# Optimization experiments

Hardware: AMD Instinct MI355X
Metric: run time of the kernel (lower is better)

Reference implementation:

```python
import jax, jax.numpy as jnp
import numpy as np

B, IN, OUT, R, G = 1024, 4096, 4096, 16, 16
N_GROUPS = IN * OUT // G  # 1048576


def setup_inputs() -> dict:
    key = jax.random.key(0)
    k1, k2, k3, k4, k5 = jax.random.split(key, 5)
    x = jax.random.normal(k1, (B, IN), dtype=jnp.float32)
    # packed 4-bit weights: each int holds two nibbles (low | high<<4), values 0..255
    qweight = jax.random.randint(k2, (N_GROUPS, G // 2), 0, 256, dtype=jnp.int32)
    # positive per-group scale (original stores abs-max as fp16, used as fp32)
    scale_factor = jax.random.uniform(k3, (N_GROUPS, 1), dtype=jnp.float32, minval=0.01, maxval=1.0)
    # kaiming-normal-ish init for lora_a; lora_b nonzero for a non-degenerate baseline
    lora_a = jax.random.normal(k4, (R, IN), dtype=jnp.float32) * np.sqrt(2.0 / IN).astype(np.float32)
    lora_b = jax.random.normal(k5, (OUT, R), dtype=jnp.float32) * 0.01
    alpha = jnp.ones((1,), dtype=jnp.float32)
    return {"x": x, "qweight": qweight, "scale_factor": scale_factor,
            "lora_a": lora_a, "lora_b": lora_b, "alpha": alpha}


def _dequantize_4bit(qweight, scale_factor):
    # qweight: [n_groups, G/2] int32 packed nibbles; scale: [n_groups, 1]
    g, half = qweight.shape
    lo = qweight & 15            # even positions
    hi = (qweight >> 4) & 15     # odd positions
    q8 = jnp.stack([lo, hi], axis=-1).reshape(g, half * 2)  # interleave -> [n_groups, G]
    x_norm = q8.astype(jnp.float32) / 15.0
    return x_norm * 2.0 * scale_factor - scale_factor       # [n_groups, G]


def reference(x, qweight, scale_factor, lora_a, lora_b, alpha):
    # dequantize and view as (in_features, -1), matching weight.view(x.shape[1], -1)
    weight = _dequantize_4bit(qweight, scale_factor).reshape(x.shape[1], -1)  # [IN, OUT]
    base = jnp.einsum('bi,oi->bo', x, weight)  # F.linear(x, weight) = x @ weight.T
    lora = alpha * jnp.einsum('br,or->bo', jnp.einsum('bi,ri->br', x, lora_a), lora_b)
    return base + lora
```

## Files before the change

kernel.cpp:

```cpp
#include <hip/hip_runtime.h>

typedef __attribute__((ext_vector_type(2))) _Float16 h2;
typedef __attribute__((ext_vector_type(2))) __fp16 p2;
typedef __attribute__((ext_vector_type(8))) _Float16 f16x8;
typedef __attribute__((ext_vector_type(4))) float fv4;
typedef __attribute__((ext_vector_type(4))) int iv4;
typedef __attribute__((ext_vector_type(2))) int iv2;
typedef unsigned int u32;

#define K_IN 4096
#define N_OUT 4096
#define KE 4160

__global__ __launch_bounds__(256) void prep_all(
        const float* __restrict__ x, const float* __restrict__ la,
        const int* __restrict__ qw, const float* __restrict__ sc,
        const float* __restrict__ lb, const float* __restrict__ alphap,
        _Float16* __restrict__ xh, _Float16* __restrict__ Wh)
{
    int bid = blockIdx.x;
    int t = threadIdx.x;
    if (bid < 1024) {
        int b = bid;
        const fv4* xp = (const fv4*)(x + (size_t)b * K_IN);
        _Float16* xr = xh + (size_t)b * KE;
        fv4 xv[4];
#pragma unroll
        for (int j = 0; j < 4; ++j) xv[j] = xp[t + j * 256];
#pragma unroll
        for (int j = 0; j < 4; ++j) {
            union { p2 h[2]; iv2 v; } u;
            u.h[0] = __builtin_amdgcn_cvt_pkrtz(xv[j].x, xv[j].y);
            u.h[1] = __builtin_amdgcn_cvt_pkrtz(xv[j].z, xv[j].w);
            *(iv2*)(xr + (size_t)(t + j * 256) * 4) = u.v;
        }
        float acc[16];
#pragma unroll
        for (int r = 0; r < 16; ++r) {
            const fv4* ap = (const fv4*)(la + (size_t)r * K_IN);
            float s = 0.f;
#pragma unroll
            for (int j = 0; j < 4; ++j) {
                fv4 av = ap[t + j * 256];
                s = fmaf(xv[j].x, av.x, s);
                s = fmaf(xv[j].y, av.y, s);
                s = fmaf(xv[j].z, av.z, s);
                s = fmaf(xv[j].w, av.w, s);
            }
            acc[r] = s;
        }
#pragma unroll
        for (int r = 0; r < 16; ++r) {
#pragma unroll
            for (int off = 1; off < 64; off <<= 1)
                acc[r] += __shfl_xor(acc[r], off);
        }
        __shared__ float red[4][16];
        int lane = t & 63, w = t >> 6;
        if (lane < 16) red[w][lane] = acc[lane];
        __syncthreads();
        if (t < 16)
            xr[4096 + t] = (_Float16)(red[0][t] + red[1][t] + red[2][t] + red[3][t]);
        else if (t < 64)
            xr[4112 + (t - 16)] = (_Float16)0.f;
    } else if (bid < 5120) {
        int grp = (bid - 1024) * 256 + t;
        int o = grp >> 8;
        int i0 = (grp & 255) << 4;
        const int* qp = qw + (size_t)grp * 8;
        iv4 q0 = *(const iv4*)qp;
        iv4 q1 = *(const iv4*)(qp + 4);
        float s = sc[grp];
        _Float16 c0h = (_Float16)(s * (2.0f / 15.0f));
        _Float16 c1h = (_Float16)(-s);
        h2 c0 = {c0h, c0h}, c1 = {c1h, c1h};
        h2 m1024 = {(_Float16)-1024.f, (_Float16)-1024.f};
        union { h2 h[4]; iv4 v; } o0, o1;
        int vals[8] = {q0.x, q0.y, q0.z, q0.w, q1.x, q1.y, q1.z, q1.w};
#pragma unroll
        for (int e = 0; e < 8; ++e) {
            unsigned wv = (unsigned)vals[e];
            unsigned qb = (wv & 15u) | ((wv & 0xF0u) << 12) | 0x64006400u;
            h2 qh;
            __builtin_memcpy(&qh, &qb, 4);
            h2 r = (qh + m1024) * c0 + c1;
            if (e < 4) o0.h[e] = r; else o1.h[e - 4] = r;
        }
        _Float16* wp = Wh + (size_t)o * KE + i0;
        *(iv4*)(wp) = o0.v;
        *(iv4*)(wp + 8) = o1.v;
    } else {
        int c = (bid - 5120) * 256 + t;
        int o = c >> 3, jj = c & 7;
        union { p2 h[4]; iv4 v; } u;
        u.v = iv4{0, 0, 0, 0};
        if (jj < 2) {
            float al = alphap[0];
            const float* wp = lb + (size_t)o * 16 + jj * 8;
#pragma unroll
            for (int e = 0; e < 4; ++e)
                u.h[e] = __builtin_amdgcn_cvt_pkrtz(al * wp[2 * e], al * wp[2 * e + 1]);
        }
        *(iv4*)(Wh + (size_t)o * KE + 4096 + jj * 8) = u.v;
    }
}

__global__ __launch_bounds__(512, 1) void qlora_gemm2(
        const _Float16* __restrict__ xh, const _Float16* __restrict__ Wh,
        float* __restrict__ out)
{
    __shared__ __align__(16) char lds[98304];

    int bid = blockIdx.x;
    int xcd = bid & 7, j = bid >> 3;
    int by = j & 7, bx = xcd * 4 + (j >> 3);
    int bm0 = by << 7, bn0 = bx << 7;

    int t = threadIdx.x;
    int lane = t & 63;
    int wid = t >> 6;
    int kg = wid & 1, wn = (wid >> 1) & 1, wm = wid >> 2;
    int rl = lane & 15, hq = lane >> 4;

    int sr = t >> 3;
    int sp = t & 7;
    int sg = sp ^ (sr & 7);
    const char* asrc[2];
    const char* bsrc[2];
#pragma unroll
    for (int i = 0; i < 2; ++i) {
        asrc[i] = (const char*)(xh + (size_t)(bm0 + i * 64 + sr) * KE) + sg * 16;
        bsrc[i] = (const char*)(Wh + (size_t)(bn0 + i * 64 + sr) * KE) + sg * 16;
    }

    auto GLOAD = [&](int ts, int buf) {
        char* Ad = lds + buf * 32768;
        char* Bd = lds + buf * 32768 + 16384;
        size_t off = (size_t)ts * 128;
#pragma unroll
        for (int i = 0; i < 2; ++i) {
            __builtin_amdgcn_global_load_lds(
                (const __attribute__((address_space(1))) u32*)(asrc[i] + off),
                (__attribute__((address_space(3))) u32*)(Ad + i * 8192 + t * 16), 16, 0, 0);
            __builtin_amdgcn_global_load_lds(
                (const __attribute__((address_space(1))) u32*)(bsrc[i] + off),
                (__attribute__((address_space(3))) u32*)(Bd + i * 8192 + t * 16), 16, 0, 0);
        }
    };

    fv4 acc[4][4];
#pragma unroll
    for (int m = 0; m < 4; ++m)
#pragma unroll
        for (int n = 0; n < 4; ++n)
            acc[m][n] = fv4{0.f, 0.f, 0.f, 0.f};

    auto COMPUTE = [&](int buf) {
        const char* As = lds + buf * 32768;
        const char* Bs = lds + buf * 32768 + 16384;
        f16x8 a[4], b[4];
        int gk = kg * 4 + hq;
        int gs = (gk ^ (rl & 7)) << 4;
#pragma unroll
        for (int m = 0; m < 4; ++m)
            a[m] = *(const f16x8*)(As + (wm * 64 + m * 16 + rl) * 128 + gs);
#pragma unroll
        for (int n = 0; n < 4; ++n)
            b[n] = *(const f16x8*)(Bs + (wn * 64 + n * 16 + rl) * 128 + gs);
        __builtin_amdgcn_s_setprio(1);
#pragma unroll
        for (int m = 0; m < 4; ++m)
#pragma unroll
            for (int n = 0; n < 4; ++n)
                acc[m][n] = __builtin_amdgcn_mfma_f32_16x16x32_f16(
                    a[m], b[n], acc[m][n], 0, 0, 0);
        __builtin_amdgcn_s_setprio(0);
    };

    GLOAD(0, 0);
    GLOAD(1, 1);
    asm volatile("s_waitcnt vmcnt(4)" ::: "memory");
    __builtin_amdgcn_s_barrier();
    __builtin_amdgcn_sched_barrier(0);

#pragma unroll 1
    for (int ts = 0; ts < 65; ++ts) {
        if (ts <= 62) GLOAD(ts + 2, (ts + 2) % 3);
        COMPUTE(ts % 3);
        if (ts <= 62) {
            asm volatile("s_waitcnt vmcnt(4)" ::: "memory");
            __builtin_amdgcn_s_barrier();
            __builtin_amdgcn_sched_barrier(0);
        } else if (ts == 63) {
            asm volatile("s_waitcnt vmcnt(0)" ::: "memory");
            __builtin_amdgcn_s_barrier();
            __builtin_amdgcn_sched_barrier(0);
        }
    }

    __syncthreads();
    if (kg == 1) {
        char* dmp = lds + (wm * 2 + wn) * 16384;
#pragma unroll
        for (int m = 0; m < 4; ++m)
#pragma unroll
            for (int n = 0; n < 4; ++n)
                *(fv4*)(dmp + (m * 4 + n) * 1024 + lane * 16) = acc[m][n];
    }
    __syncthreads();
    if (kg == 0) {
        const char* dmp = lds + (wm * 2 + wn) * 16384;
#pragma unroll
        for (int m = 0; m < 4; ++m) {
            int row0 = bm0 + wm * 64 + m * 16 + hq * 4;
#pragma unroll
            for (int n = 0; n < 4; ++n) {
                fv4 p = *(const fv4*)(dmp + (m * 4 + n) * 1024 + lane * 16);
                fv4 v = acc[m][n];
                v.x += p.x; v.y += p.y; v.z += p.z; v.w += p.w;
                int col = bn0 + wn * 64 + n * 16 + rl;
#pragma unroll
                for (int r = 0; r < 4; ++r)
                    out[(size_t)(row0 + r) * N_OUT + col] = v[r];
            }
        }
    }
}

extern "C" void kernel_launch(void* const* d_in, const int* in_sizes, int n_in,
                              void* d_out, int out_size, void* d_ws, size_t ws_size,
                              hipStream_t stream) {
    const float* x  = (const float*)d_in[0];
    const int*   qw = (const int*)d_in[1];
    const float* sc = (const float*)d_in[2];
    const float* la = (const float*)d_in[3];
    const float* lb = (const float*)d_in[4];
    const float* al = (const float*)d_in[5];
    float* out = (float*)d_out;

    const size_t WH_BYTES = (size_t)N_OUT * KE * 2;
    _Float16* Wh = (_Float16*)d_ws;
    _Float16* xh = (_Float16*)((char*)d_ws + WH_BYTES);
    (void)ws_size; (void)n_in; (void)in_sizes; (void)out_size;

    prep_all<<<5248, 256, 0, stream>>>(x, la, qw, sc, lb, al, xh, Wh);
    qlora_gemm2<<<256, 512, 0, stream>>>(xh, Wh, out);
}
```

Measured before the change: 69.75 us.

## Pre-pack operands into MFMA fragment layout and load directly to registers

The prep kernel now writes x and the dequantized weights in a fragment-major packed layout (16-row blocks, 8-half groups), so each lane's MFMA operand is one contiguous 16-byte global load. The GEMM drops the LDS staging buffers, the triple-buffered global_load_lds pipeline and its barriers, and instead double-buffers register fragments loaded straight from global memory. This removes LDS traffic and synchronisation. In exchange there is no cross-wave data sharing, so each tile is fetched from L2 by several waves, and latency hiding depends on having only one fragment in flight.

```diff
diff --git a/kernel.cpp b/kernel.cpp
--- a/kernel.cpp
+++ b/kernel.cpp
@@ -6,33 +6,36 @@
 typedef __attribute__((ext_vector_type(4))) float fv4;
 typedef __attribute__((ext_vector_type(4))) int iv4;
 typedef __attribute__((ext_vector_type(2))) int iv2;
-typedef unsigned int u32;
 
 #define K_IN 4096
 #define N_OUT 4096
 #define KE 4160
+#define NG 520
+
 
 __global__ __launch_bounds__(256) void prep_all(
         const float* __restrict__ x, const float* __restrict__ la,
         const int* __restrict__ qw, const float* __restrict__ sc,
         const float* __restrict__ lb, const float* __restrict__ alphap,
-        _Float16* __restrict__ xh, _Float16* __restrict__ Wh)
+        _Float16* __restrict__ xp, _Float16* __restrict__ Wp)
 {
     int bid = blockIdx.x;
     int t = threadIdx.x;
     if (bid < 1024) {
         int b = bid;
-        const fv4* xp = (const fv4*)(x + (size_t)b * K_IN);
-        _Float16* xr = xh + (size_t)b * KE;
+        int rb = b >> 4, rl = b & 15;
+        const fv4* xv4 = (const fv4*)(x + (size_t)b * K_IN);
         fv4 xv[4];
 #pragma unroll
-        for (int j = 0; j < 4; ++j) xv[j] = xp[t + j * 256];
+        for (int j = 0; j < 4; ++j) xv[j] = xv4[t + j * 256];
 #pragma unroll
         for (int j = 0; j < 4; ++j) {
+            int idx = t + j * 256;
+            int g = idx >> 1, sub = (idx & 1) * 4;
             union { p2 h[2]; iv2 v; } u;
             u.h[0] = __builtin_amdgcn_cvt_pkrtz(xv[j].x, xv[j].y);
             u.h[1] = __builtin_amdgcn_cvt_pkrtz(xv[j].z, xv[j].w);
-            *(iv2*)(xr + (size_t)(t + j * 256) * 4) = u.v;
+            *(iv2*)(xp + (((size_t)rb * NG + g) * 16 + rl) * 8 + sub) = u.v;
         }
         float acc[16];
 #pragma unroll
@@ -59,18 +62,19 @@
         int lane = t & 63, w = t >> 6;
         if (lane < 16) red[w][lane] = acc[lane];
         __syncthreads();
-        if (t < 16)
-            xr[4096 + t] = (_Float16)(red[0][t] + red[1][t] + red[2][t] + red[3][t]);
-        else if (t < 64)
-            xr[4112 + (t - 16)] = (_Float16)0.f;
+        if (t < 64) {
+            float v = (t < 16) ? (red[0][t] + red[1][t] + red[2][t] + red[3][t]) : 0.f;
+            int g = 512 + (t >> 3), e = t & 7;
+            xp[(((size_t)rb * NG + g) * 16 + rl) * 8 + e] = (_Float16)v;
+        }
     } else if (bid < 5120) {
-        int grp = (bid - 1024) * 256 + t;
-        int o = grp >> 8;
-        int i0 = (grp & 255) << 4;
-        const int* qp = qw + (size_t)grp * 8;
+        int o = bid - 1024;
+        int gi = t;
+        int cb = o >> 4, rl = o & 15;
+        const int* qp = qw + ((size_t)o * 256 + gi) * 8;
         iv4 q0 = *(const iv4*)qp;
         iv4 q1 = *(const iv4*)(qp + 4);
-        float s = sc[grp];
+        float s = sc[(size_t)o * 256 + gi];
         _Float16 c0h = (_Float16)(s * (2.0f / 15.0f));
         _Float16 c1h = (_Float16)(-s);
         h2 c0 = {c0h, c0h}, c1 = {c1h, c1h};
@@ -86,12 +90,13 @@
             h2 r = (qh + m1024) * c0 + c1;
             if (e < 4) o0.h[e] = r; else o1.h[e - 4] = r;
         }
-        _Float16* wp = Wh + (size_t)o * KE + i0;
-        *(iv4*)(wp) = o0.v;
-        *(iv4*)(wp + 8) = o1.v;
+        _Float16* w0 = Wp + (((size_t)cb * NG + 2 * gi) * 16 + rl) * 8;
+        *(iv4*)(w0) = o0.v;
+        *(iv4*)(w0 + 128) = o1.v;
     } else {
         int c = (bid - 5120) * 256 + t;
         int o = c >> 3, jj = c & 7;
+        int cb = o >> 4, rl = o & 15;
         union { p2 h[4]; iv4 v; } u;
         u.v = iv4{0, 0, 0, 0};
         if (jj < 2) {
@@ -101,15 +106,15 @@
             for (int e = 0; e < 4; ++e)
                 u.h[e] = __builtin_amdgcn_cvt_pkrtz(al * wp[2 * e], al * wp[2 * e + 1]);
         }
-        *(iv4*)(Wh + (size_t)o * KE + 4096 + jj * 8) = u.v;
+        *(iv4*)(Wp + (((size_t)cb * NG + 512 + jj) * 16 + rl) * 8) = u.v;
     }
 }
 
 __global__ __launch_bounds__(512, 1) void qlora_gemm2(
-        const _Float16* __restrict__ xh, const _Float16* __restrict__ Wh,
+        const _Float16* __restrict__ xp, const _Float16* __restrict__ Wp,
         float* __restrict__ out)
 {
-    __shared__ __align__(16) char lds[98304];
+    __shared__ __align__(16) char lds[65536];
 
     int bid = blockIdx.x;
     int xcd = bid & 7, j = bid >> 3;
@@ -122,30 +127,28 @@
     int kg = wid & 1, wn = (wid >> 1) & 1, wm = wid >> 2;
     int rl = lane & 15, hq = lane >> 4;
 
-    int sr = t >> 3;
-    int sp = t & 7;
-    int sg = sp ^ (sr & 7);
-    const char* asrc[2];
-    const char* bsrc[2];
-#pragma unroll
-    for (int i = 0; i < 2; ++i) {
-        asrc[i] = (const char*)(xh + (size_t)(bm0 + i * 64 + sr) * KE) + sg * 16;
-        bsrc[i] = (const char*)(Wh + (size_t)(bn0 + i * 64 + sr) * KE) + sg * 16;
-    }
-
-    auto GLOAD = [&](int ts, int buf) {
-        char* Ad = lds + buf * 32768;
-        char* Bd = lds + buf * 32768 + 16384;
-        size_t off = (size_t)ts * 128;
-#pragma unroll
-        for (int i = 0; i < 2; ++i) {
-            __builtin_amdgcn_global_load_lds(
-                (const __attribute__((address_space(1))) u32*)(asrc[i] + off),
-                (__attribute__((address_space(3))) u32*)(Ad + i * 8192 + t * 16), 16, 0, 0);
-            __builtin_amdgcn_global_load_lds(
-                (const __attribute__((address_space(1))) u32*)(bsrc[i] + off),
-                (__attribute__((address_space(3))) u32*)(Bd + i * 8192 + t * 16), 16, 0, 0);
-        }
+    const char* abase[4];
+    const char* bbase[4];
+#pragma unroll
+    for (int m = 0; m < 4; ++m) {
+        int rb = by * 8 + wm * 4 + m;
+        abase[m] = (const char*)xp + (((size_t)rb * NG + kg * 4 + hq) * 16 + rl) * 16;
+    }
+#pragma unroll
+    for (int n = 0; n < 4; ++n) {
+        int cb = bx * 8 + wn * 4 + n;
+        bbase[n] = (const char*)Wp + (((size_t)cb * NG + kg * 4 + hq) * 16 + rl) * 16;
+    }
+
+    struct Frag { iv4 a[4]; iv4 b[4]; };
+    Frag fA, fB;
+
+    auto LOADF = [&](Frag& f, int ts) {
+        size_t off = (size_t)ts * 2048;
+#pragma unroll
+        for (int m = 0; m < 4; ++m) f.a[m] = *(const iv4*)(abase[m] + off);
+#pragma unroll
+        for (int n = 0; n < 4; ++n) f.b[n] = *(const iv4*)(bbase[n] + off);
     };
 
     fv4 acc[4][4];
@@ -155,48 +158,31 @@
         for (int n = 0; n < 4; ++n)
             acc[m][n] = fv4{0.f, 0.f, 0.f, 0.f};
 
-    auto COMPUTE = [&](int buf) {
-        const char* As = lds + buf * 32768;
-        const char* Bs = lds + buf * 32768 + 16384;
-        f16x8 a[4], b[4];
-        int gk = kg * 4 + hq;
-        int gs = (gk ^ (rl & 7)) << 4;
-#pragma unroll
-        for (int m = 0; m < 4; ++m)
-            a[m] = *(const f16x8*)(As + (wm * 64 + m * 16 + rl) * 128 + gs);
-#pragma unroll
-        for (int n = 0; n < 4; ++n)
-            b[n] = *(const f16x8*)(Bs + (wn * 64 + n * 16 + rl) * 128 + gs);
+    auto MFMAF = [&](const Frag& f) {
+        union { iv4 v; f16x8 h; } ua[4], ub[4];
+#pragma unroll
+        for (int m = 0; m < 4; ++m) ua[m].v = f.a[m];
+#pragma unroll
+        for (int n = 0; n < 4; ++n) ub[n].v = f.b[n];
         __builtin_amdgcn_s_setprio(1);
 #pragma unroll
         for (int m = 0; m < 4; ++m)
 #pragma unroll
             for (int n = 0; n < 4; ++n)
                 acc[m][n] = __builtin_amdgcn_mfma_f32_16x16x32_f16(
-                    a[m], b[n], acc[m][n], 0, 0, 0);
+                    ua[m].h, ub[n].h, acc[m][n], 0, 0, 0);
         __builtin_amdgcn_s_setprio(0);
     };
 
-    GLOAD(0, 0);
-    GLOAD(1, 1);
-    asm volatile("s_waitcnt vmcnt(4)" ::: "memory");
-    __builtin_amdgcn_s_barrier();
-    __builtin_amdgcn_sched_barrier(0);
-
+    LOADF(fA, 0);
 #pragma unroll 1
-    for (int ts = 0; ts < 65; ++ts) {
-        if (ts <= 62) GLOAD(ts + 2, (ts + 2) % 3);
-        COMPUTE(ts % 3);
-        if (ts <= 62) {
-            asm volatile("s_waitcnt vmcnt(4)" ::: "memory");
-            __builtin_amdgcn_s_barrier();
-            __builtin_amdgcn_sched_barrier(0);
-        } else if (ts == 63) {
-            asm volatile("s_waitcnt vmcnt(0)" ::: "memory");
-            __builtin_amdgcn_s_barrier();
-            __builtin_amdgcn_sched_barrier(0);
-        }
-    }
+    for (int ts = 0; ts < 64; ts += 2) {
+        LOADF(fB, ts + 1);
+        MFMAF(fA);
+        LOADF(fA, ts + 2);
+        MFMAF(fB);
+    }
+    MFMAF(fA);
 
     __syncthreads();
     if (kg == 1) {
@@ -238,11 +224,11 @@
     const float* al = (const float*)d_in[5];
     float* out = (float*)d_out;
 
-    const size_t WH_BYTES = (size_t)N_OUT * KE * 2;
-    _Float16* Wh = (_Float16*)d_ws;
-    _Float16* xh = (_Float16*)((char*)d_ws + WH_BYTES);
+    const size_t WP_BYTES = (size_t)(N_OUT / 16) * NG * 16 * 16;
+    _Float16* Wp = (_Float16*)d_ws;
+    _Float16* xp = (_Float16*)((char*)d_ws + WP_BYTES);
     (void)ws_size; (void)n_in; (void)in_sizes; (void)out_size;
 
-    prep_all<<<5248, 256, 0, stream>>>(x, la, qw, sc, lb, al, xh, Wh);
-    qlora_gemm2<<<256, 512, 0, stream>>>(xh, Wh, out);
+    prep_all<<<5248, 256, 0, stream>>>(x, la, qw, sc, lb, al, xp, Wp);
+    qlora_gemm2<<<256, 512, 0, stream>>>(xp, Wp, out);
 }
```

After: 91.21 us. +30.8%, slower.
